# Kernel optimization log

Measured on AMD Instinct MI355X. Metric: run time of the kernel, lower is better.

Reference implementation:

```python
import jax, jax.numpy as jnp
import numpy as np

DT = 0.02
B = 524288
HID = 128


def setup_inputs() -> dict:
    key = jax.random.key(0)
    ks = jax.random.split(key, 11)
    def lin_init(k, fan_in, fan_out):
        # torch nn.Linear default: U(-1/sqrt(fan_in), 1/sqrt(fan_in))
        bound = 1.0 / np.sqrt(fan_in)
        kw, kb = jax.random.split(k)
        W = jax.random.uniform(kw, (fan_in, fan_out), jnp.float32, -bound, bound)
        b = jax.random.uniform(kb, (fan_out,), jnp.float32, -bound, bound)
        return W, b
    W1, b1 = lin_init(ks[0], 2, HID)
    W2, b2 = lin_init(ks[1], HID, HID)
    W3, b3 = lin_init(ks[2], HID, HID)
    W4, b4 = lin_init(ks[3], HID, 1)
    return {
        "q": jax.random.normal(ks[4], (B, 1), jnp.float32),
        "p": jax.random.normal(ks[5], (B, 1), jnp.float32),
        "F_ext": jax.random.normal(ks[6], (B, 1), jnp.float32),
        "W1": W1, "b1": b1, "W2": W2, "b2": b2,
        "W3": W3, "b3": b3, "W4": W4, "b4": b4,
    }


def reference(q, p, F_ext, W1, b1, W2, b2, W3, b3, W4, b4):
    def H_sum(q, p):
        s = jnp.concatenate([q, p], axis=1)          # [B, 2]
        h = jnp.tanh(s @ W1 + b1)                    # [B, 128]
        h = jnp.tanh(h @ W2 + b2)
        h = jnp.tanh(h @ W3 + b3)
        return jnp.sum(h @ W4 + b4)                  # scalar; samples independent
    dH_dq, dH_dp = jax.grad(H_sum, argnums=(0, 1))(q, p)
    dq_dt = dH_dp
    dp_dt = -dH_dq + F_ext
    return jnp.concatenate([dq_dt * DT, dp_dt * DT], axis=1)  # [B, 2]
```

## Files before the change

### kernel.cpp

```cpp
#include <hip/hip_runtime.h>

#define DT 0.02f

typedef __attribute__((ext_vector_type(8))) __bf16 bf16x8;
typedef __attribute__((ext_vector_type(4))) __bf16 bf16x4;
typedef __attribute__((ext_vector_type(4))) float  f32x4;

__device__ __forceinline__ float fast_tanh(float x){
    float e = __builtin_amdgcn_exp2f(x * 2.8853900817779268f);
    return 1.0f - 2.0f * __builtin_amdgcn_rcpf(e + 1.0f);
}
__device__ __forceinline__ char* ldsx(char* base, int m, int j){
    return base + (((m << 8) + (j << 1)) ^ ((m & 7) << 4));
}

template<int MODE>
__device__ __forceinline__ void hnn_gemm(const __bf16* __restrict__ Wg,
                                         char* Xbuf, char* Obuf,
                                         const float* __restrict__ bias,
                                         const float* __restrict__ W1,
                                         const float* __restrict__ b1,
                                         const float* __restrict__ qv,
                                         const float* __restrict__ pv,
                                         int w, int l)
{
    const int lr = l & 15, lg = l >> 4;
    const int rbase = w * 32;

    f32x4 acc[2][4];
    #pragma unroll
    for (int mt = 0; mt < 2; ++mt)
        #pragma unroll
        for (int nt = 0; nt < 4; ++nt) acc[mt][nt] = 0.0f;

    #pragma unroll
    for (int ks = 0; ks < 4; ++ks){
        const int kb = ks * 32 + lg * 8;
        bf16x8 a[2], b[4];
        #pragma unroll
        for (int mt = 0; mt < 2; ++mt)
            a[mt] = *(const bf16x8*)(Wg + ((rbase + mt * 16 + lr) << 7) + kb);
        #pragma unroll
        for (int nt = 0; nt < 4; ++nt)
            b[nt] = *(const bf16x8*)ldsx(Xbuf, nt * 16 + lr, kb);
        #pragma unroll
        for (int mt = 0; mt < 2; ++mt)
            #pragma unroll
            for (int nt = 0; nt < 4; ++nt)
                acc[mt][nt] = __builtin_amdgcn_mfma_f32_16x16x32_bf16(
                    a[mt], b[nt], acc[mt][nt], 0, 0, 0);
    }

    if (MODE == 1){
        #pragma unroll
        for (int mt = 0; mt < 2; ++mt){
            const int j0 = rbase + mt * 16 + lg * 4;
            const f32x4 bv = *(const f32x4*)(bias + j0);
            #pragma unroll
            for (int nt = 0; nt < 4; ++nt){
                const int m = nt * 16 + lr;
                bf16x4 hv;
                #pragma unroll
                for (int jr = 0; jr < 4; ++jr)
                    hv[jr] = (__bf16)fast_tanh(acc[mt][nt][jr] + bv[jr]);
                *(bf16x4*)ldsx(Obuf, m, j0) = hv;
            }
        }
    } else if (MODE == 0){
        #pragma unroll
        for (int mt = 0; mt < 2; ++mt){
            const int j0 = rbase + mt * 16 + lg * 4;
            #pragma unroll
            for (int nt = 0; nt < 4; ++nt){
                const int m = nt * 16 + lr;
                bf16x4* hp = (bf16x4*)ldsx(Obuf, m, j0);
                bf16x4 hv = *hp, gv;
                #pragma unroll
                for (int jr = 0; jr < 4; ++jr){
                    float h = (float)hv[jr];
                    gv[jr] = (__bf16)(acc[mt][nt][jr] * (1.0f - h * h));
                }
                *hp = gv;
            }
        }
    } else {
        float qq[4], pp[4];
        #pragma unroll
        for (int nt = 0; nt < 4; ++nt){
            qq[nt] = qv[nt * 16 + lr];
            pp[nt] = pv[nt * 16 + lr];
        }
        #pragma unroll
        for (int mt = 0; mt < 2; ++mt){
            const int j0 = rbase + mt * 16 + lg * 4;
            const f32x4 wq = *(const f32x4*)(W1 + j0);
            const f32x4 wp = *(const f32x4*)(W1 + 128 + j0);
            const f32x4 bb = *(const f32x4*)(b1 + j0);
            #pragma unroll
            for (int nt = 0; nt < 4; ++nt){
                const int m = nt * 16 + lr;
                bf16x4 gv;
                #pragma unroll
                for (int jr = 0; jr < 4; ++jr){
                    float h = fast_tanh(fmaf(qq[nt], wq[jr], fmaf(pp[nt], wp[jr], bb[jr])));
                    gv[jr] = (__bf16)(acc[mt][nt][jr] * (1.0f - h * h));
                }
                *(bf16x4*)ldsx(Obuf, m, j0) = gv;
            }
        }
    }
}

__global__ void hnn_prep(const float* __restrict__ W2, const float* __restrict__ W3,
                         __bf16* __restrict__ ws)
{
    int idx = blockIdx.x * 256 + threadIdx.x;
    int k = idx >> 7, n = idx & 127;
    __bf16 v2 = (__bf16)W2[idx];
    __bf16 v3 = (__bf16)W3[idx];
    ws[n * 128 + k]         = v2;
    ws[16384 + n * 128 + k] = v3;
    ws[32768 + idx]         = v2;
    ws[49152 + idx]         = v3;
}

__global__ __launch_bounds__(256, 4)
void hnn_main(const float* __restrict__ q, const float* __restrict__ p,
              const float* __restrict__ Fx,
              const float* __restrict__ W1, const float* __restrict__ b1,
              const float* __restrict__ b2, const float* __restrict__ b3,
              const float* __restrict__ W4,
              const __bf16* __restrict__ ws,
              float* __restrict__ out)
{
    __shared__ char bufA[16384];
    __shared__ char bufB[16384];
    const int t = threadIdx.x;
    const int w = t >> 6, l = t & 63;
    const int lr = l & 15, lg = l >> 4;
    const long mg0 = (long)blockIdx.x * 64;

    {
        const int j0 = lr * 8;
        f32x4 wq0 = *(const f32x4*)(W1 + j0),       wq1 = *(const f32x4*)(W1 + j0 + 4);
        f32x4 wp0 = *(const f32x4*)(W1 + 128 + j0), wp1 = *(const f32x4*)(W1 + 128 + j0 + 4);
        f32x4 bb0 = *(const f32x4*)(b1 + j0),       bb1 = *(const f32x4*)(b1 + j0 + 4);
        #pragma unroll
        for (int i = 0; i < 4; ++i){
            int m = w * 16 + i * 4 + lg;
            float qq = q[mg0 + m], pp = p[mg0 + m];
            bf16x8 hv;
            #pragma unroll
            for (int u = 0; u < 4; ++u){
                hv[u]     = (__bf16)fast_tanh(fmaf(qq, wq0[u], fmaf(pp, wp0[u], bb0[u])));
                hv[4 + u] = (__bf16)fast_tanh(fmaf(qq, wq1[u], fmaf(pp, wp1[u], bb1[u])));
            }
            *(bf16x8*)ldsx(bufA, m, j0) = hv;
        }
    }
    __syncthreads();
    hnn_gemm<1>(ws,         bufA, bufB, b2, nullptr, nullptr, nullptr, nullptr, w, l);
    __syncthreads();
    hnn_gemm<1>(ws + 16384, bufB, bufA, b3, nullptr, nullptr, nullptr, nullptr, w, l);
    __syncthreads();

    {
        const int j0 = lr * 8;
        f32x4 w40 = *(const f32x4*)(W4 + j0), w41 = *(const f32x4*)(W4 + j0 + 4);
        #pragma unroll
        for (int i = 0; i < 4; ++i){
            int m = w * 16 + i * 4 + lg;
            bf16x8* ptr = (bf16x8*)ldsx(bufA, m, j0);
            bf16x8 hv = *ptr, gv;
            #pragma unroll
            for (int u = 0; u < 4; ++u){
                float h0 = (float)hv[u],     h1v = (float)hv[4 + u];
                gv[u]     = (__bf16)(w40[u] * (1.0f - h0 * h0));
                gv[4 + u] = (__bf16)(w41[u] * (1.0f - h1v * h1v));
            }
            *ptr = gv;
        }
    }
    __syncthreads();
    hnn_gemm<0>(ws + 49152, bufA, bufB, nullptr, nullptr, nullptr, nullptr, nullptr, w, l);
    __syncthreads();
    hnn_gemm<2>(ws + 32768, bufB, bufA, nullptr, W1, b1, q + mg0, p + mg0, w, l);
    __syncthreads();

    {
        const int m = t & 63, q4 = t >> 6;
        float sdq = 0.f, sdp = 0.f;
        #pragma unroll
        for (int i = 0; i < 4; ++i){
            int j0 = q4 * 32 + i * 8;
            bf16x8 gv = *(const bf16x8*)ldsx(bufA, m, j0);
            f32x4 wq0 = *(const f32x4*)(W1 + j0),       wq1 = *(const f32x4*)(W1 + j0 + 4);
            f32x4 wp0 = *(const f32x4*)(W1 + 128 + j0), wp1 = *(const f32x4*)(W1 + 128 + j0 + 4);
            #pragma unroll
            for (int u = 0; u < 4; ++u){
                float g0 = (float)gv[u], g1v = (float)gv[4 + u];
                sdq = fmaf(g0, wq0[u], fmaf(g1v, wq1[u], sdq));
                sdp = fmaf(g0, wp0[u], fmaf(g1v, wp1[u], sdp));
            }
        }
        float2* red = (float2*)bufB;
        red[m * 4 + q4] = make_float2(sdq, sdp);
    }
    __syncthreads();
    if (t < 64){
        const float2* red = (const float2*)bufB;
        float2 r0 = red[t * 4 + 0], r1 = red[t * 4 + 1];
        float2 r2 = red[t * 4 + 2], r3 = red[t * 4 + 3];
        float dq = r0.x + r1.x + r2.x + r3.x;
        float dp = r0.y + r1.y + r2.y + r3.y;
        long gm = mg0 + t;
        float2 o;
        o.x = DT * dp;
        o.y = DT * (-dq + Fx[gm]);
        *(float2*)(out + gm * 2) = o;
    }
}

extern "C" void kernel_launch(void* const* d_in, const int* in_sizes, int n_in,
                              void* d_out, int out_size, void* d_ws, size_t ws_size,
                              hipStream_t stream) {
    const float* q   = (const float*)d_in[0];
    const float* p   = (const float*)d_in[1];
    const float* Fx  = (const float*)d_in[2];
    const float* W1  = (const float*)d_in[3];
    const float* b1  = (const float*)d_in[4];
    const float* W2  = (const float*)d_in[5];
    const float* b2  = (const float*)d_in[6];
    const float* W3  = (const float*)d_in[7];
    const float* b3  = (const float*)d_in[8];
    const float* W4  = (const float*)d_in[9];
    __bf16* ws = (__bf16*)d_ws;
    float* out = (float*)d_out;

    (void)in_sizes; (void)n_in; (void)out_size; (void)ws_size;

    hnn_prep<<<64, 256, 0, stream>>>(W2, W3, ws);
    hnn_main<<<8192, 256, 0, stream>>>(q, p, Fx, W1, b1, b2, b3, W4, ws, out);
}
```

Measured before the change: 238.9 us.

## Fuse W4 backprop into layer-3 epilogue and keep layer-1 tanh derivative in registers

Layer 1 is now computed in the same MFMA fragment layout as the GEMM outputs, so each thread keeps its layer-1 tanh derivative (1-h^2) in bf16 registers. The final backward GEMM multiplies by that saved mask instead of recomputing tanh from q, p, W1 and b1. The W4 gradient seed is folded into the layer-3 GEMM epilogue, which removes one LDS read/modify/write pass and one barrier. In exchange each thread holds 8 more bf16x4 registers, which could hurt occupancy, and the layer-1 LDS stores use a different access pattern.

Measured after the change: 234.1 us. 1.02x faster.

```diff
diff --git a/kernel.cpp b/kernel.cpp
--- a/kernel.cpp
+++ b/kernel.cpp
@@ -18,10 +18,8 @@
 __device__ __forceinline__ void hnn_gemm(const __bf16* __restrict__ Wg,
                                          char* Xbuf, char* Obuf,
                                          const float* __restrict__ bias,
-                                         const float* __restrict__ W1,
-                                         const float* __restrict__ b1,
-                                         const float* __restrict__ qv,
-                                         const float* __restrict__ pv,
+                                         const float* __restrict__ w4,
+                                         const bf16x4 (*m1)[4],
                                          int w, int l)
 {
     const int lr = l & 15, lg = l >> 4;
@@ -64,6 +62,24 @@
                 for (int jr = 0; jr < 4; ++jr)
                     hv[jr] = (__bf16)fast_tanh(acc[mt][nt][jr] + bv[jr]);
                 *(bf16x4*)ldsx(Obuf, m, j0) = hv;
+            }
+        }
+    } else if (MODE == 4){
+        #pragma unroll
+        for (int mt = 0; mt < 2; ++mt){
+            const int j0 = rbase + mt * 16 + lg * 4;
+            const f32x4 bv = *(const f32x4*)(bias + j0);
+            const f32x4 wv = *(const f32x4*)(w4 + j0);
+            #pragma unroll
+            for (int nt = 0; nt < 4; ++nt){
+                const int m = nt * 16 + lr;
+                bf16x4 gv;
+                #pragma unroll
+                for (int jr = 0; jr < 4; ++jr){
+                    float tt = fast_tanh(acc[mt][nt][jr] + bv[jr]);
+                    gv[jr] = (__bf16)(wv[jr] * (1.0f - tt * tt));
+                }
+                *(bf16x4*)ldsx(Obuf, m, j0) = gv;
             }
         }
     } else if (MODE == 0){
@@ -84,27 +100,17 @@
             }
         }
     } else {
-        float qq[4], pp[4];
-        #pragma unroll
-        for (int nt = 0; nt < 4; ++nt){
-            qq[nt] = qv[nt * 16 + lr];
-            pp[nt] = pv[nt * 16 + lr];
-        }
-        #pragma unroll
-        for (int mt = 0; mt < 2; ++mt){
-            const int j0 = rbase + mt * 16 + lg * 4;
-            const f32x4 wq = *(const f32x4*)(W1 + j0);
-            const f32x4 wp = *(const f32x4*)(W1 + 128 + j0);
-            const f32x4 bb = *(const f32x4*)(b1 + j0);
-            #pragma unroll
-            for (int nt = 0; nt < 4; ++nt){
-                const int m = nt * 16 + lr;
+        #pragma unroll
+        for (int mt = 0; mt < 2; ++mt){
+            const int j0 = rbase + mt * 16 + lg * 4;
+            #pragma unroll
+            for (int nt = 0; nt < 4; ++nt){
+                const int m = nt * 16 + lr;
+                const bf16x4 mv = m1[mt][nt];
                 bf16x4 gv;
                 #pragma unroll
-                for (int jr = 0; jr < 4; ++jr){
-                    float h = fast_tanh(fmaf(qq[nt], wq[jr], fmaf(pp[nt], wp[jr], bb[jr])));
-                    gv[jr] = (__bf16)(acc[mt][nt][jr] * (1.0f - h * h));
-                }
+                for (int jr = 0; jr < 4; ++jr)
+                    gv[jr] = (__bf16)(acc[mt][nt][jr] * (float)mv[jr]);
                 *(bf16x4*)ldsx(Obuf, m, j0) = gv;
             }
         }
@@ -140,51 +146,43 @@
     const int lr = l & 15, lg = l >> 4;
     const long mg0 = (long)blockIdx.x * 64;
 
+    bf16x4 mask1[2][4];
     {
-        const int j0 = lr * 8;
-        f32x4 wq0 = *(const f32x4*)(W1 + j0),       wq1 = *(const f32x4*)(W1 + j0 + 4);
-        f32x4 wp0 = *(const f32x4*)(W1 + 128 + j0), wp1 = *(const f32x4*)(W1 + 128 + j0 + 4);
-        f32x4 bb0 = *(const f32x4*)(b1 + j0),       bb1 = *(const f32x4*)(b1 + j0 + 4);
-        #pragma unroll
-        for (int i = 0; i < 4; ++i){
-            int m = w * 16 + i * 4 + lg;
-            float qq = q[mg0 + m], pp = p[mg0 + m];
-            bf16x8 hv;
-            #pragma unroll
-            for (int u = 0; u < 4; ++u){
-                hv[u]     = (__bf16)fast_tanh(fmaf(qq, wq0[u], fmaf(pp, wp0[u], bb0[u])));
-                hv[4 + u] = (__bf16)fast_tanh(fmaf(qq, wq1[u], fmaf(pp, wp1[u], bb1[u])));
-            }
-            *(bf16x8*)ldsx(bufA, m, j0) = hv;
-        }
-    }
-    __syncthreads();
-    hnn_gemm<1>(ws,         bufA, bufB, b2, nullptr, nullptr, nullptr, nullptr, w, l);
-    __syncthreads();
-    hnn_gemm<1>(ws + 16384, bufB, bufA, b3, nullptr, nullptr, nullptr, nullptr, w, l);
-    __syncthreads();
-
-    {
-        const int j0 = lr * 8;
-        f32x4 w40 = *(const f32x4*)(W4 + j0), w41 = *(const f32x4*)(W4 + j0 + 4);
-        #pragma unroll
-        for (int i = 0; i < 4; ++i){
-            int m = w * 16 + i * 4 + lg;
-            bf16x8* ptr = (bf16x8*)ldsx(bufA, m, j0);
-            bf16x8 hv = *ptr, gv;
-            #pragma unroll
-            for (int u = 0; u < 4; ++u){
-                float h0 = (float)hv[u],     h1v = (float)hv[4 + u];
-                gv[u]     = (__bf16)(w40[u] * (1.0f - h0 * h0));
-                gv[4 + u] = (__bf16)(w41[u] * (1.0f - h1v * h1v));
-            }
-            *ptr = gv;
-        }
-    }
-    __syncthreads();
-    hnn_gemm<0>(ws + 49152, bufA, bufB, nullptr, nullptr, nullptr, nullptr, nullptr, w, l);
-    __syncthreads();
-    hnn_gemm<2>(ws + 32768, bufB, bufA, nullptr, W1, b1, q + mg0, p + mg0, w, l);
+        const int rbase = w * 32;
+        float qq[4], pp[4];
+        #pragma unroll
+        for (int nt = 0; nt < 4; ++nt){
+            qq[nt] = q[mg0 + nt * 16 + lr];
+            pp[nt] = p[mg0 + nt * 16 + lr];
+        }
+        #pragma unroll
+        for (int mt = 0; mt < 2; ++mt){
+            const int j0 = rbase + mt * 16 + lg * 4;
+            const f32x4 wq = *(const f32x4*)(W1 + j0);
+            const f32x4 wp = *(const f32x4*)(W1 + 128 + j0);
+            const f32x4 bb = *(const f32x4*)(b1 + j0);
+            #pragma unroll
+            for (int nt = 0; nt < 4; ++nt){
+                bf16x4 hv, mv;
+                #pragma unroll
+                for (int jr = 0; jr < 4; ++jr){
+                    float h = fast_tanh(fmaf(qq[nt], wq[jr], fmaf(pp[nt], wp[jr], bb[jr])));
+                    hv[jr] = (__bf16)h;
+                    mv[jr] = (__bf16)(1.0f - h * h);
+                }
+                *(bf16x4*)ldsx(bufA, nt * 16 + lr, j0) = hv;
+                mask1[mt][nt] = mv;
+            }
+        }
+    }
+    __syncthreads();
+    hnn_gemm<1>(ws,         bufA, bufB, b2, nullptr, nullptr, w, l);
+    __syncthreads();
+    hnn_gemm<4>(ws + 16384, bufB, bufA, b3, W4, nullptr, w, l);
+    __syncthreads();
+    hnn_gemm<0>(ws + 49152, bufA, bufB, nullptr, nullptr, nullptr, w, l);
+    __syncthreads();
+    hnn_gemm<5>(ws + 32768, bufB, bufA, nullptr, nullptr, mask1, w, l);
     __syncthreads();
 
     {
```
